# Optimization experiments

Measured on AMD Instinct MI355X. Metric: run time of the kernel, lower is better.

Reference implementation:

```python
import jax, jax.numpy as jnp
import numpy as np
from jax import lax

# static config (matches init_kwargs / input_specs)
B, T, DUR = 16, 256, 4
MEL = T * DUR                      # 1024 frames; durations rows each sum to MEL
D, H, DH, L = 512, 8, 64, 4
INTER, K, OUT = 2048, 3, 80
VOCAB, MAXLEN = 256, 4096


def _sincos(maxlen, d):
    den = jnp.exp(-jnp.arange(0, d, 2).astype(jnp.float32) * (np.log(10000.0) / d))
    ang = jnp.arange(maxlen, dtype=jnp.float32)[:, None] * den[None, :]
    return jnp.stack([jnp.sin(ang), jnp.cos(ang)], axis=-1).reshape(maxlen, d)


def _ln(x, g, b):
    m = jnp.mean(x, -1, keepdims=True)
    v = jnp.mean((x - m) ** 2, -1, keepdims=True)
    return (x - m) * lax.rsqrt(v + 1e-5) * g + b


def _layer(x, am, wqkv, bqkv, wo, bo, ln1g, ln1b, c1w, c1b, c2w, c2b, ln2g, ln2b):
    bs, s, _ = x.shape
    qkv = (x @ wqkv + bqkv).reshape(bs, s, 3, H, DH)
    q, k, v = qkv[:, :, 0], qkv[:, :, 1], qkv[:, :, 2]
    scores = jnp.einsum('bqhd,bkhd->bhqk', q, k) / np.sqrt(DH).astype(np.float32)
    scores = scores + am[:, None, None, :]          # additive key mask (-inf padded)
    attn = jax.nn.softmax(scores, axis=-1)
    ctx = jnp.einsum('bhqk,bkhd->bqhd', attn, v).reshape(bs, s, H * DH)
    x = _ln(x + ctx @ wo + bo, ln1g, ln1b)
    h = lax.conv_general_dilated(x, c1w, (1,), 'SAME', dimension_numbers=('NLC', 'LIO', 'NLC')) + c1b
    h = jax.nn.relu(h)
    h = lax.conv_general_dilated(h, c2w, (1,), 'SAME', dimension_numbers=('NLC', 'LIO', 'NLC')) + c2b
    return _ln(x + h, ln2g, ln2b)


def _stack(x, am, params):
    for i in range(L):
        x = _layer(x, am, *(p[i] for p in params))
    return x


def setup_inputs() -> dict:
    key = jax.random.key(0)
    ks = iter(jax.random.split(key, 64))

    def nrm(shape, s=0.02):
        return jax.random.normal(next(ks), shape, jnp.float32) * s

    inp = {
        'tokens': jax.random.randint(next(ks), (B, T), 0, VOCAB),
        'token_lengths': jax.random.randint(next(ks), (B,), T // 2, T),
        'melspec_length': jax.random.randint(next(ks), (B,), MEL // 2, MEL),
        'durations': jnp.full((B, T), DUR, jnp.int32),   # rows sum to MEL (module assert)
        'mel_len': MEL,
        'emb': nrm((VOCAB, D), 1.0),
    }
    for pre in ('enc', 'dec'):
        inp[pre + '_wqkv'] = nrm((L, D, 3 * H * DH))
        inp[pre + '_bqkv'] = jnp.zeros((L, 3 * H * DH))
        inp[pre + '_wo'] = nrm((L, H * DH, D))
        inp[pre + '_bo'] = jnp.zeros((L, D))
        inp[pre + '_ln1g'] = jnp.ones((L, D))
        inp[pre + '_ln1b'] = jnp.zeros((L, D))
        inp[pre + '_c1w'] = nrm((L, K, D, INTER))
        inp[pre + '_c1b'] = jnp.zeros((L, INTER))
        inp[pre + '_c2w'] = nrm((L, K, INTER, D))
        inp[pre + '_c2b'] = jnp.zeros((L, D))
        inp[pre + '_ln2g'] = jnp.ones((L, D))
        inp[pre + '_ln2b'] = jnp.zeros((L, D))
    inp['out_w'] = nrm((D, OUT))
    inp['out_b'] = jnp.zeros((OUT,))
    return inp


def reference(tokens, token_lengths, melspec_length, durations, mel_len, emb,
              enc_wqkv, enc_bqkv, enc_wo, enc_bo, enc_ln1g, enc_ln1b,
              enc_c1w, enc_c1b, enc_c2w, enc_c2b, enc_ln2g, enc_ln2b,
              dec_wqkv, dec_bqkv, dec_wo, dec_bo, dec_ln1g, dec_ln1b,
              dec_c1w, dec_c1b, dec_c2w, dec_c2b, dec_ln2g, dec_ln2b,
              out_w, out_b):
    bs, t = tokens.shape
    pos = _sincos(MAXLEAN := MAXLEN, D)
    x = emb[tokens]
    # faithful to original: x + (x + pos_embedding[:bs]) where pos buffer is [maxlen,1,D]
    x = 2.0 * x + pos[:bs][:, None, :]
    am = jnp.where(jnp.arange(t)[None, :] > token_lengths[:, None], -jnp.inf, 0.0)
    enc = _stack(x, am, (enc_wqkv, enc_bqkv, enc_wo, enc_bo, enc_ln1g, enc_ln1b,
                         enc_c1w, enc_c1b, enc_c2w, enc_c2b, enc_ln2g, enc_ln2b))
    # length regulator: equivalent gather form of mask.T @ encoder (O(MEL*D) not O(T*MEL*D))
    cums = jnp.cumsum(durations, axis=1)
    frames = jnp.arange(mel_len)
    idx = jax.vmap(lambda c: jnp.searchsorted(c, frames, side='right'))(cums)  # [B, MEL]
    dec_in = jnp.take_along_axis(enc, idx[:, :, None], axis=1)
    keep = (frames[None, :] <= melspec_length[:, None]).astype(dec_in.dtype)
    dec_in = dec_in * keep[:, :, None]
    am2 = jnp.where(frames[None, :] > melspec_length[:, None], -jnp.inf, 0.0)
    dec = _stack(dec_in, am2, (dec_wqkv, dec_bqkv, dec_wo, dec_bo, dec_ln1g, dec_ln1b,
                               dec_c1w, dec_c1b, dec_c2w, dec_c2b, dec_ln2g, dec_ln2b))
    out = dec @ out_w + out_b                      # [B, MEL, OUT]
    return jnp.transpose(out, (0, 2, 1))           # [B, OUT, MEL]
```

## Files before the change

kernel.cpp:

```cpp
#include <hip/hip_runtime.h>

typedef unsigned short u16;
typedef short short8 __attribute__((ext_vector_type(8)));
typedef float floatx4 __attribute__((ext_vector_type(4)));

static constexpr int CB = 16, CT = 256, CMEL = 1024, CD = 512, CH = 8, CDH = 64, CL = 4;
static constexpr int CINTER = 2048, COUT = 80;
static constexpr int CQKV = 3 * CH * CDH;

static __device__ __forceinline__ float bf2f(u16 u) {
  union { unsigned u; float f; } v; v.u = ((unsigned)u) << 16; return v.f;
}
static __device__ __forceinline__ u16 f2bf(float f) {
  union { float f; unsigned u; } v; v.f = f;
  unsigned r = v.u + 0x7fffu + ((v.u >> 16) & 1u);
  return (u16)(r >> 16);
}

static __device__ __forceinline__ void gld16(const u16* g, u16* lds) {
  __builtin_amdgcn_global_load_lds((const __attribute__((address_space(1))) void*)g,
                                   (__attribute__((address_space(3))) void*)lds, 16, 0, 0);
}

template<int NT, bool RELU>
__global__ __launch_bounds__(512)
void gemm2_k(const u16* __restrict__ A, const u16* __restrict__ Bm,
             u16* __restrict__ Cm, const float* __restrict__ bias,
             int M, int N, int K, int lda, int ldb, int ldc,
             int Sm1, long tapStrideB, const u16* __restrict__ zp)
{
  constexpr int BM = 256, BN = 128;
  constexpr int H = (NT == 3) ? 8 : 0;
  constexpr int AR = BM + 2 * H;
  __shared__ u16 As[AR * 32];
  __shared__ u16 Bs[NT * BN * 32];

  const int t = threadIdx.x;
  const int lane = t & 63;
  const int wave = t >> 6;
  const int wrow = wave >> 1;
  const int wcol = wave & 1;
  const int bn0 = blockIdx.x * BN;
  const int bm0 = blockIdx.y * BM;

  floatx4 acc[4][4];
#pragma unroll
  for (int i = 0; i < 4; ++i)
#pragma unroll
    for (int j = 0; j < 4; ++j) acc[i][j] = (floatx4){0.f, 0.f, 0.f, 0.f};

  const int rsub = lane >> 2;
  const int g8 = (((lane & 3) ^ ((lane >> 3) & 3)) << 3);

  const u16* aP0; const u16* aP1; const u16* aP2 = nullptr;
  {
    int gg0 = bm0 - H + wave * 16 + rsub;
    int gg1 = bm0 - H + (wave + 8) * 16 + rsub;
    aP0 = ((NT == 1) || ((unsigned)gg0 < (unsigned)M)) ? A + (long)gg0 * lda + g8 : nullptr;
    aP1 = ((NT == 1) || ((unsigned)gg1 < (unsigned)M)) ? A + (long)gg1 * lda + g8 : nullptr;
    if (NT == 3 && wave == 0) {
      int gg2 = bm0 - H + 256 + rsub;
      aP2 = ((unsigned)gg2 < (unsigned)M) ? A + (long)gg2 * lda + g8 : nullptr;
    }
  }
  const int aL0 = wave * 512, aL1 = (wave + 8) * 512, aL2 = 16 * 512;

  const u16* bP[NT]; int bL[NT];
#pragma unroll
  for (int i = 0; i < NT; ++i) {
    bP[i] = Bm + (long)i * tapStrideB + (long)(bn0 + wave * 16 + rsub) * ldb + g8;
    bL[i] = (i * BN + wave * 16) * 32;
  }

  const int q = lane >> 4, fm = lane & 15;
  const int swzB = (q ^ ((fm >> 1) & 3)) << 3;
  int swzA[NT];
  bool mv[NT][4];
#pragma unroll
  for (int tap = 0; tap < NT; ++tap) {
    const int dlt = tap - ((NT == 3) ? 1 : 0);
    swzA[tap] = (q ^ ((((H + dlt + fm) & 15) >> 1) & 3)) << 3;
#pragma unroll
    for (int i = 0; i < 4; ++i) {
      int s = (bm0 + wrow * 64 + i * 16 + fm) & Sm1;
      mv[tap][i] = ((unsigned)(s + dlt) <= (unsigned)Sm1);
    }
  }
  const short8 zero8 = {};

  for (int k0 = 0; k0 < K; k0 += 32) {
    gld16(aP0 ? aP0 + k0 : zp, &As[aL0]);
    gld16(aP1 ? aP1 + k0 : zp, &As[aL1]);
    if (NT == 3 && wave == 0) gld16(aP2 ? aP2 + k0 : zp, &As[aL2]);
#pragma unroll
    for (int i = 0; i < NT; ++i) gld16(bP[i] + k0, &Bs[bL[i]]);
    __syncthreads();

#pragma unroll
    for (int tap = 0; tap < NT; ++tap) {
      const int dlt = tap - ((NT == 3) ? 1 : 0);
      short8 af[4], bfr[4];
#pragma unroll
      for (int i = 0; i < 4; ++i) {
        af[i] = *(const short8*)&As[(wrow * 64 + i * 16 + fm + H + dlt) * 32 + swzA[tap]];
        if (NT == 3 && !mv[tap][i]) af[i] = zero8;
      }
#pragma unroll
      for (int j = 0; j < 4; ++j)
        bfr[j] = *(const short8*)&Bs[(tap * BN + wcol * 64 + j * 16 + fm) * 32 + swzB];
#pragma unroll
      for (int i = 0; i < 4; ++i)
#pragma unroll
        for (int j = 0; j < 4; ++j)
          acc[i][j] = __builtin_amdgcn_mfma_f32_16x16x32_bf16(af[i], bfr[j], acc[i][j], 0, 0, 0);
    }
    __syncthreads();
  }

  const int rbase = bm0 + wrow * 64 + ((lane >> 4) << 2);
  const int cbase = bn0 + wcol * 64 + fm;
#pragma unroll
  for (int j = 0; j < 4; ++j) {
    int col = cbase + j * 16;
    float bv = bias ? bias[col] : 0.f;
#pragma unroll
    for (int i = 0; i < 4; ++i) {
#pragma unroll
      for (int r = 0; r < 4; ++r) {
        int row = rbase + i * 16 + r;
        float v = acc[i][j][r] + bv;
        if (RELU) v = fmaxf(v, 0.f);
        Cm[(long)row * ldc + col] = f2bf(v);
      }
    }
  }
}

__global__ __launch_bounds__(512)
void attn_k(const u16* __restrict__ qkv, const u16* __restrict__ vt,
            u16* __restrict__ ctx, const int* __restrict__ lens, int S)
{
  __shared__ u16 Ks[2][64 * 32];
  __shared__ u16 Vts[2][64 * 32];
  __shared__ u16 Ps[8][16][80];

  const int t = threadIdx.x, lane = t & 63, w = t >> 6;
  const int bh = blockIdx.y, b = bh >> 3, h = bh & 7;
  const int q0 = blockIdx.x * 128;
  const int len = lens[b];
  const int fm = lane & 15, quad = lane >> 4;
  const int swz8 = ((quad ^ ((fm >> 1) & 3)) << 3);
  const int rsub = lane >> 2;
  const int g8 = (((lane & 3) ^ ((lane >> 3) & 3)) << 3);

  const int qrow = q0 + w * 16 + fm;
  short8 bq[2];
  bq[0] = *(const short8*)&qkv[(long)(b * S + qrow) * CQKV + h * 64 + quad * 8];
  bq[1] = *(const short8*)&qkv[(long)(b * S + qrow) * CQKV + h * 64 + 32 + quad * 8];

  const int ksW = w & 1, rg = (w >> 1) & 3;
  const u16* kBase = qkv + ((long)b * S + rg * 16 + rsub) * CQKV + CD + h * 64 + ksW * 32 + g8;
  const u16* vBase = vt + ((long)bh * 64 + rg * 16 + rsub) * S + ksW * 32 + g8;
  u16* kDst = &Ks[ksW][rg * 512];
  u16* vDst = &Vts[ksW][rg * 512];

  floatx4 acc_o[4];
#pragma unroll
  for (int j = 0; j < 4; ++j) acc_o[j] = (floatx4){0.f, 0.f, 0.f, 0.f};
  float m = -1e30f, l = 0.f;

  for (int kv0 = 0; kv0 < S; kv0 += 64) {
    __syncthreads();
    gld16(kBase + (long)kv0 * CQKV, kDst);
    gld16(vBase + kv0, vDst);
    __syncthreads();

    floatx4 sa[4];
#pragma unroll
    for (int i = 0; i < 4; ++i) sa[i] = (floatx4){0.f, 0.f, 0.f, 0.f};
#pragma unroll
    for (int ks = 0; ks < 2; ++ks) {
#pragma unroll
      for (int mi = 0; mi < 4; ++mi) {
        short8 ak = *(const short8*)&Ks[ks][(mi * 16 + fm) * 32 + swz8];
        sa[mi] = __builtin_amdgcn_mfma_f32_16x16x32_bf16(ak, bq[ks], sa[mi], 0, 0, 0);
      }
    }

    float p[4][4], tm = -1e30f;
#pragma unroll
    for (int mi = 0; mi < 4; ++mi)
#pragma unroll
      for (int r = 0; r < 4; ++r) {
        int kvg = kv0 + mi * 16 + quad * 4 + r;
        float v = (kvg <= len) ? sa[mi][r] * 0.125f : -1e30f;
        p[mi][r] = v; tm = fmaxf(tm, v);
      }
    tm = fmaxf(tm, __shfl_xor(tm, 16));
    tm = fmaxf(tm, __shfl_xor(tm, 32));
    const float mnew = fmaxf(m, tm);
    const float al = __expf(m - mnew);
    float ts = 0.f;
#pragma unroll
    for (int mi = 0; mi < 4; ++mi)
#pragma unroll
      for (int r = 0; r < 4; ++r) { float e = __expf(p[mi][r] - mnew); p[mi][r] = e; ts += e; }
    ts += __shfl_xor(ts, 16);
    ts += __shfl_xor(ts, 32);
    l = l * al + ts; m = mnew;
    float al4[4];
#pragma unroll
    for (int r = 0; r < 4; ++r) al4[r] = __shfl(al, ((lane >> 4) << 2) + r, 64);
#pragma unroll
    for (int j = 0; j < 4; ++j)
#pragma unroll
      for (int r = 0; r < 4; ++r) acc_o[j][r] *= al4[r];

#pragma unroll
    for (int mi = 0; mi < 4; ++mi) {
      unsigned u01 = (unsigned)f2bf(p[mi][0]) | ((unsigned)f2bf(p[mi][1]) << 16);
      unsigned u23 = (unsigned)f2bf(p[mi][2]) | ((unsigned)f2bf(p[mi][3]) << 16);
      *(uint2*)&Ps[w][fm][mi * 16 + quad * 4] = make_uint2(u01, u23);
    }

#pragma unroll
    for (int ks = 0; ks < 2; ++ks) {
      short8 ap = *(const short8*)&Ps[w][fm][ks * 32 + quad * 8];
#pragma unroll
      for (int nj = 0; nj < 4; ++nj) {
        short8 bv = *(const short8*)&Vts[ks][(nj * 16 + fm) * 32 + swz8];
        acc_o[nj] = __builtin_amdgcn_mfma_f32_16x16x32_bf16(ap, bv, acc_o[nj], 0, 0, 0);
      }
    }
  }

  float li4[4];
#pragma unroll
  for (int r = 0; r < 4; ++r) li4[r] = 1.f / __shfl(l, ((lane >> 4) << 2) + r, 64);
#pragma unroll
  for (int nj = 0; nj < 4; ++nj)
#pragma unroll
    for (int r = 0; r < 4; ++r) {
      int qr = q0 + w * 16 + quad * 4 + r;
      ctx[(long)(b * S + qr) * CD + h * 64 + nj * 16 + fm] = f2bf(acc_o[nj][r] * li4[r]);
    }
}

template<int BM, int BN>
__global__ __launch_bounds__(256)
void gemmF_k(const u16* __restrict__ A, const u16* __restrict__ Bm,
             float* __restrict__ Cm, const float* __restrict__ bias,
             int M, int N, int K, int lda, int ldb,
             const u16* __restrict__ zp)
{
  __shared__ u16 As[BM * 32];
  __shared__ u16 Bs[BN * 32];

  const int t = threadIdx.x;
  const int lane = t & 63;
  const int wave = t >> 6;
  constexpr int WCOLS = BN / 64;
  const int wrow = wave / WCOLS;
  const int wcol = wave % WCOLS;
  const int bn0 = blockIdx.x * BN;
  const int bm0 = blockIdx.y * BM;

  floatx4 acc[4][4];
#pragma unroll
  for (int i = 0; i < 4; ++i)
#pragma unroll
    for (int j = 0; j < 4; ++j) acc[i][j] = (floatx4){0.f, 0.f, 0.f, 0.f};

  const int rsub = lane >> 2;
  const int g8 = (((lane & 3) ^ ((lane >> 3) & 3)) << 3);
  constexpr int PA = BM / 64, PB = BN / 64;

  const int q = lane >> 4, fm = lane & 15;
  const int swz8 = ((q ^ ((fm >> 1) & 3)) << 3);

  const u16* aP[PA]; const u16* bP[PB];
#pragma unroll
  for (int p = 0; p < PA; ++p)
    aP[p] = A + (long)(bm0 + p * 64 + wave * 16 + rsub) * lda + g8;
#pragma unroll
  for (int p = 0; p < PB; ++p) {
    int r = p * 64 + wave * 16 + rsub;
    bP[p] = ((bn0 + r) < N) ? (Bm + (long)(bn0 + r) * ldb + g8) : nullptr;
  }

  for (int k0 = 0; k0 < K; k0 += 32) {
#pragma unroll
    for (int p = 0; p < PA; ++p)
      gld16(aP[p] + k0, &As[(p * 64 + wave * 16) * 32]);
#pragma unroll
    for (int p = 0; p < PB; ++p)
      gld16(bP[p] ? bP[p] + k0 : zp, &Bs[(p * 64 + wave * 16) * 32]);
    __syncthreads();

    short8 af[4], bfr[4];
#pragma unroll
    for (int i = 0; i < 4; ++i)
      af[i] = *(const short8*)&As[(wrow * 64 + i * 16 + fm) * 32 + swz8];
#pragma unroll
    for (int j = 0; j < 4; ++j)
      bfr[j] = *(const short8*)&Bs[(wcol * 64 + j * 16 + fm) * 32 + swz8];
#pragma unroll
    for (int i = 0; i < 4; ++i)
#pragma unroll
      for (int j = 0; j < 4; ++j)
        acc[i][j] = __builtin_amdgcn_mfma_f32_16x16x32_bf16(af[i], bfr[j], acc[i][j], 0, 0, 0);
    __syncthreads();
  }

  const int rbase = bm0 + wrow * 64 + ((lane >> 4) << 2);
  const int cbase = bn0 + wcol * 64 + (lane & 15);
#pragma unroll
  for (int j = 0; j < 4; ++j) {
    int col = cbase + j * 16;
    if (col >= N) continue;
    float bv = bias ? bias[col] : 0.f;
#pragma unroll
    for (int i = 0; i < 4; ++i) {
#pragma unroll
      for (int r = 0; r < 4; ++r) {
        int row = rbase + i * 16 + r;
        Cm[((long)(row >> 10) * COUT + col) * CMEL + (row & 1023)] = acc[i][j][r] + bv;
      }
    }
  }
}

__global__ void cvt_t_k(const float* __restrict__ src, u16* __restrict__ dst, int K, int N)
{
  const int tap = blockIdx.z;
  const int n0 = blockIdx.x * 32, k0 = blockIdx.y * 32;
  __shared__ float tile[32][33];
  const int t = threadIdx.x;
  const int c = t & 31, rr = t >> 5;
  const float* s = src + (long)tap * K * N;
  u16* d = dst + (long)tap * K * N;
#pragma unroll
  for (int i = 0; i < 4; ++i) {
    int k = k0 + rr + i * 8, n = n0 + c;
    tile[rr + i * 8][c] = (k < K && n < N) ? s[(long)k * N + n] : 0.f;
  }
  __syncthreads();
#pragma unroll
  for (int i = 0; i < 4; ++i) {
    int n = n0 + rr + i * 8, k = k0 + c;
    if (n < N && k < K) d[(long)n * K + k] = f2bf(tile[c][rr + i * 8]);
  }
}

__global__ void vtr_k(const u16* __restrict__ qkv, u16* __restrict__ vt, int S)
{
  const int s0 = blockIdx.x * 64;
  const int bh = blockIdx.y;
  const int b = bh >> 3, h = bh & 7;
  __shared__ u16 tile[64][65];
  const int t = threadIdx.x;
  const int wave = t >> 6, lane = t & 63;
#pragma unroll
  for (int i = 0; i < 16; ++i) {
    int sl = wave * 16 + i;
    tile[sl][lane] = qkv[(long)(b * S + s0 + sl) * CQKV + 2 * CD + h * 64 + lane];
  }
  __syncthreads();
  const int dl = t >> 2, sc4 = (t & 3) << 4;
  u16* dstp = vt + ((long)bh * 64 + dl) * S + s0 + sc4;
  short8 v0, v1;
#pragma unroll
  for (int j = 0; j < 8; ++j) { v0[j] = (short)tile[sc4 + j][dl]; v1[j] = (short)tile[sc4 + 8 + j][dl]; }
  *(short8*)dstp = v0;
  *(short8*)(dstp + 8) = v1;
}

__global__ void fill_k(float* __restrict__ o, int n, float v)
{
  int i = blockIdx.x * 256 + threadIdx.x;
  if (i < n) o[i] = v;
}

__global__ void embed_k(const int* __restrict__ tok, const float* __restrict__ emb,
                        u16* __restrict__ X)
{
  const long idx = (long)blockIdx.x * 256 + threadIdx.x;
  const int d = (int)(idx & (CD - 1));
  const int m = (int)(idx >> 9);
  const int b = m >> 8;
  const float e = emb[(long)tok[m] * CD + d];
  const int i2 = d >> 1;
  const float den = __expf(-(float)(2 * i2) * (9.210340371976184f / 512.f));
  const float ang = (float)b * den;
  const float p = (d & 1) ? __cosf(ang) : __sinf(ang);
  X[idx] = f2bf(2.f * e + p);
}

__global__ void ln_res_k(const u16* __restrict__ X, const u16* __restrict__ Y,
                         const float* __restrict__ g, const float* __restrict__ bta,
                         u16* __restrict__ O)
{
  const int m = blockIdx.x, t = threadIdx.x;
  const long base = (long)m * CD;
  float v0 = bf2f(X[base + t]) + bf2f(Y[base + t]);
  float v1 = bf2f(X[base + t + 256]) + bf2f(Y[base + t + 256]);
  __shared__ float red[256];
  red[t] = v0 + v1; __syncthreads();
  for (int s = 128; s > 0; s >>= 1) { if (t < s) red[t] += red[t + s]; __syncthreads(); }
  const float mean = red[0] * (1.f / 512.f);
  __syncthreads();
  const float d0 = v0 - mean, d1 = v1 - mean;
  red[t] = d0 * d0 + d1 * d1; __syncthreads();
  for (int s = 128; s > 0; s >>= 1) { if (t < s) red[t] += red[t + s]; __syncthreads(); }
  const float rstd = rsqrtf(red[0] * (1.f / 512.f) + 1e-5f);
  O[base + t]       = f2bf(d0 * rstd * g[t] + bta[t]);
  O[base + t + 256] = f2bf(d1 * rstd * g[t + 256] + bta[t + 256]);
}

__global__ void cumsum_k(const int* __restrict__ dur, int* __restrict__ cums)
{
  int b = threadIdx.x;
  if (b < CB) {
    int s = 0;
    for (int t = 0; t < CT; ++t) { s += dur[b * CT + t]; cums[b * CT + t] = s; }
  }
}

__global__ void regulate_k(const u16* __restrict__ xe, const int* __restrict__ cums,
                           const int* __restrict__ mlen, u16* __restrict__ xd)
{
  const int m = blockIdx.x;
  const int b = m >> 10, f = m & (CMEL - 1);
  int lo = 0, hi = CT;
  while (lo < hi) { int mid = (lo + hi) >> 1; if (cums[b * CT + mid] <= f) lo = mid + 1; else hi = mid; }
  const int idx = min(lo, CT - 1);
  const bool keep = (f <= mlen[b]);
  const u16* src = xe + ((long)b * CT + idx) * CD;
  u16* dst = xd + (long)m * CD;
  const int t = threadIdx.x;
  dst[t]       = keep ? src[t] : (u16)0;
  dst[t + 256] = keep ? src[t + 256] : (u16)0;
}

extern "C" void kernel_launch(void* const* d_in, const int* in_sizes, int n_in,
                              void* d_out, int out_size, void* d_ws, size_t ws_size,
                              hipStream_t stream)
{
  (void)in_sizes; (void)n_in;
  const int*   tokens = (const int*)d_in[0];
  const int*   tlen   = (const int*)d_in[1];
  const int*   mlen   = (const int*)d_in[2];
  const int*   dur    = (const int*)d_in[3];
  const float* emb    = (const float*)d_in[5];
  const float* ew[12]; const float* dw[12];
  for (int i = 0; i < 12; ++i) { ew[i] = (const float*)d_in[6 + i]; dw[i] = (const float*)d_in[18 + i]; }
  const float* out_w = (const float*)d_in[30];
  const float* out_b = (const float*)d_in[31];

  const int Me = CB * CT;
  const int Md = CB * CMEL;

  const size_t SZ_ZP   = 256;
  const size_t SZ_WBUF = (size_t)3 * CD * CINTER * 2;
  const size_t SZ_XE   = (size_t)Me * CD * 2;
  const size_t SZ_XD   = (size_t)Md * CD * 2;
  const size_t SZ_QKV  = (size_t)Md * CQKV * 2;
  const size_t SZ_HB   = (size_t)Md * CINTER * 2;
  const size_t SZ_CUMS = (size_t)CB * CT * 4;
  auto al = [](size_t b) { return (b + 255) & ~(size_t)255; };
  size_t U = al(SZ_QKV) > al(SZ_HB) ? al(SZ_QKV) : al(SZ_HB);
  size_t total = al(SZ_ZP) + al(SZ_WBUF) + al(SZ_XE) + 3 * al(SZ_XD) + U + al(SZ_CUMS);
  if (total > ws_size) {
    fill_k<<<dim3((unsigned)((out_size + 255) / 256)), dim3(256), 0, stream>>>(
        (float*)d_out, out_size, 1000.0f);
    return;
  }

  char* p = (char*)d_ws;
  auto take = [&](size_t bytes) { char* r = p; p += al(bytes); return r; };
  u16*  zp   = (u16*)take(SZ_ZP);
  u16*  wbuf = (u16*)take(SZ_WBUF);
  u16*  xe   = (u16*)take(SZ_XE);
  u16*  xd   = (u16*)take(SZ_XD);
  u16*  x1   = (u16*)take(SZ_XD);
  u16*  yb   = (u16*)take(SZ_XD);
  char* U0   = take(U);
  u16*  qkvB = (u16*)U0;
  u16*  hb   = (u16*)U0;
  int* cums = (int*)take(SZ_CUMS);

  hipMemsetAsync(zp, 0, SZ_ZP, stream);

  auto cvtT = [&](const float* s, u16* d, int K, int N, int taps) {
    cvt_t_k<<<dim3((unsigned)((N + 31) / 32), (unsigned)((K + 31) / 32), (unsigned)taps),
              dim3(256), 0, stream>>>(s, d, K, N);
  };

  embed_k<<<dim3((unsigned)((long)Me * CD / 256)), dim3(256), 0, stream>>>(tokens, emb, xe);

  auto run_stack = [&](u16* x, int S, int M, const int* lens, const float* const* W) {
    u16* vt = yb;
    for (int l = 0; l < CL; ++l) {
      cvtT(W[0] + (long)l * CD * CQKV, wbuf, CD, CQKV, 1);
      gemm2_k<1, false><<<dim3(CQKV / 128, M / 256), dim3(512), 0, stream>>>(
          x, wbuf, qkvB, W[1] + l * CQKV, M, CQKV, CD, CD, CD, CQKV, S - 1, 0, zp);
      vtr_k<<<dim3((unsigned)(S / 64), (unsigned)(CB * CH)), dim3(256), 0, stream>>>(qkvB, vt, S);
      attn_k<<<dim3((unsigned)(S / 128), (unsigned)(CB * CH)), dim3(512), 0, stream>>>(
          qkvB, vt, x1, lens, S);
      cvtT(W[2] + (long)l * CD * CD, wbuf, CD, CD, 1);
      gemm2_k<1, false><<<dim3(CD / 128, M / 256), dim3(512), 0, stream>>>(
          x1, wbuf, yb, W[3] + l * CD, M, CD, CD, CD, CD, CD, S - 1, 0, zp);
      ln_res_k<<<dim3((unsigned)M), dim3(256), 0, stream>>>(x, yb, W[4] + l * CD, W[5] + l * CD, x1);
      cvtT(W[6] + (long)l * 3 * CD * CINTER, wbuf, CD, CINTER, 3);
      gemm2_k<3, true><<<dim3(CINTER / 128, M / 256), dim3(512), 0, stream>>>(
          x1, wbuf, hb, W[7] + l * CINTER, M, CINTER, CD, CD, CD, CINTER,
          S - 1, (long)CD * CINTER, zp);
      cvtT(W[8] + (long)l * 3 * CINTER * CD, wbuf, CINTER, CD, 3);
      gemm2_k<3, false><<<dim3(CD / 128, M / 256), dim3(512), 0, stream>>>(
          hb, wbuf, yb, W[9] + l * CD, M, CD, CINTER, CINTER, CINTER, CD,
          S - 1, (long)CINTER * CD, zp);
      ln_res_k<<<dim3((unsigned)M), dim3(256), 0, stream>>>(x1, yb, W[10] + l * CD, W[11] + l * CD, x);
    }
  };

  run_stack(xe, CT, Me, tlen, ew);

  cumsum_k<<<dim3(1), dim3(64), 0, stream>>>(dur, cums);
  regulate_k<<<dim3((unsigned)(CB * CMEL)), dim3(256), 0, stream>>>(xe, cums, mlen, xd);

  run_stack(xd, CMEL, Md, mlen, dw);

  cvtT(out_w, wbuf, CD, COUT, 1);
  gemmF_k<128, 128><<<dim3(1, Md / 128), dim3(256), 0, stream>>>(
      xd, wbuf, (float*)d_out, out_b, Md, COUT, CD, CD, CD, zp);
}
```

Baseline: 2.891 ms.

## Halve GEMM row tile to 128 and widen attention KV tile to 128

The conv/projection GEMM drops from 256x128 tiles with 512 threads to 128x128 tiles with 256 threads, so each thread now loads two B rows per tap. This doubles the grid size to improve occupancy and load balance, at the cost of less A/B reuse per tile. The attention kernel now processes 128 keys per iteration instead of 64, halving the number of sync/load rounds and softmax rescales. The price is more registers per thread and larger LDS buffers.

Result: faster. 2.679 ms (-7.3%).

```diff
diff --git a/kernel.cpp b/kernel.cpp
--- a/kernel.cpp
+++ b/kernel.cpp
@@ -23,13 +23,13 @@
 }
 
 template<int NT, bool RELU>
-__global__ __launch_bounds__(512)
+__global__ __launch_bounds__(256)
 void gemm2_k(const u16* __restrict__ A, const u16* __restrict__ Bm,
              u16* __restrict__ Cm, const float* __restrict__ bias,
              int M, int N, int K, int lda, int ldb, int ldc,
              int Sm1, long tapStrideB, const u16* __restrict__ zp)
 {
-  constexpr int BM = 256, BN = 128;
+  constexpr int BM = 128, BN = 128;
   constexpr int H = (NT == 3) ? 8 : 0;
   constexpr int AR = BM + 2 * H;
   __shared__ u16 As[AR * 32];
@@ -55,22 +55,25 @@
   const u16* aP0; const u16* aP1; const u16* aP2 = nullptr;
   {
     int gg0 = bm0 - H + wave * 16 + rsub;
-    int gg1 = bm0 - H + (wave + 8) * 16 + rsub;
+    int gg1 = bm0 - H + (wave + 4) * 16 + rsub;
     aP0 = ((NT == 1) || ((unsigned)gg0 < (unsigned)M)) ? A + (long)gg0 * lda + g8 : nullptr;
     aP1 = ((NT == 1) || ((unsigned)gg1 < (unsigned)M)) ? A + (long)gg1 * lda + g8 : nullptr;
     if (NT == 3 && wave == 0) {
-      int gg2 = bm0 - H + 256 + rsub;
+      int gg2 = bm0 - H + 128 + rsub;
       aP2 = ((unsigned)gg2 < (unsigned)M) ? A + (long)gg2 * lda + g8 : nullptr;
     }
   }
-  const int aL0 = wave * 512, aL1 = (wave + 8) * 512, aL2 = 16 * 512;
-
-  const u16* bP[NT]; int bL[NT];
-#pragma unroll
-  for (int i = 0; i < NT; ++i) {
-    bP[i] = Bm + (long)i * tapStrideB + (long)(bn0 + wave * 16 + rsub) * ldb + g8;
-    bL[i] = (i * BN + wave * 16) * 32;
-  }
+  const int aL0 = wave * 512, aL1 = (wave + 4) * 512, aL2 = 8 * 512;
+
+  const u16* bP[NT][2]; int bL[NT][2];
+#pragma unroll
+  for (int i = 0; i < NT; ++i)
+#pragma unroll
+    for (int j = 0; j < 2; ++j) {
+      int r = (wave + j * 4) * 16 + rsub;
+      bP[i][j] = Bm + (long)i * tapStrideB + (long)(bn0 + r) * ldb + g8;
+      bL[i][j] = (i * BN + (wave + j * 4) * 16) * 32;
+    }
 
   const int q = lane >> 4, fm = lane & 15;
   const int swzB = (q ^ ((fm >> 1) & 3)) << 3;
@@ -93,7 +96,9 @@
     gld16(aP1 ? aP1 + k0 : zp, &As[aL1]);
     if (NT == 3 && wave == 0) gld16(aP2 ? aP2 + k0 : zp, &As[aL2]);
 #pragma unroll
-    for (int i = 0; i < NT; ++i) gld16(bP[i] + k0, &Bs[bL[i]]);
+    for (int i = 0; i < NT; ++i)
+#pragma unroll
+      for (int j = 0; j < 2; ++j) gld16(bP[i][j] + k0, &Bs[bL[i][j]]);
     __syncthreads();
 
 #pragma unroll
@@ -140,9 +145,9 @@
 void attn_k(const u16* __restrict__ qkv, const u16* __restrict__ vt,
             u16* __restrict__ ctx, const int* __restrict__ lens, int S)
 {
-  __shared__ u16 Ks[2][64 * 32];
-  __shared__ u16 Vts[2][64 * 32];
-  __shared__ u16 Ps[8][16][80];
+  __shared__ __attribute__((aligned(16))) u16 Ks[2][128 * 32];
+  __shared__ __attribute__((aligned(16))) u16 Vts[4][64 * 32];
+  __shared__ __attribute__((aligned(16))) u16 Ps[8][16][136];
 
   const int t = threadIdx.x, lane = t & 63, w = t >> 6;
   const int bh = blockIdx.y, b = bh >> 3, h = bh & 7;
@@ -158,38 +163,46 @@
   bq[0] = *(const short8*)&qkv[(long)(b * S + qrow) * CQKV + h * 64 + quad * 8];
   bq[1] = *(const short8*)&qkv[(long)(b * S + qrow) * CQKV + h * 64 + 32 + quad * 8];
 
-  const int ksW = w & 1, rg = (w >> 1) & 3;
-  const u16* kBase = qkv + ((long)b * S + rg * 16 + rsub) * CQKV + CD + h * 64 + ksW * 32 + g8;
-  const u16* vBase = vt + ((long)bh * 64 + rg * 16 + rsub) * S + ksW * 32 + g8;
-  u16* kDst = &Ks[ksW][rg * 512];
-  u16* vDst = &Vts[ksW][rg * 512];
+  const int ksW = w & 1, rgA = w >> 1, rgB = (w >> 1) + 4;
+  const u16* kBaseA = qkv + ((long)b * S + rgA * 16 + rsub) * CQKV + CD + h * 64 + ksW * 32 + g8;
+  const u16* kBaseB = qkv + ((long)b * S + rgB * 16 + rsub) * CQKV + CD + h * 64 + ksW * 32 + g8;
+  u16* kDstA = &Ks[ksW][rgA * 512];
+  u16* kDstB = &Ks[ksW][rgB * 512];
+  const int kvs0 = (2 * w) >> 2, dhc0 = (2 * w) & 3;
+  const int kvs1 = (2 * w + 1) >> 2, dhc1 = (2 * w + 1) & 3;
+  const u16* vBase0 = vt + ((long)bh * 64 + dhc0 * 16 + rsub) * S + kvs0 * 32 + g8;
+  const u16* vBase1 = vt + ((long)bh * 64 + dhc1 * 16 + rsub) * S + kvs1 * 32 + g8;
+  u16* vDst0 = &Vts[kvs0][dhc0 * 512];
+  u16* vDst1 = &Vts[kvs1][dhc1 * 512];
 
   floatx4 acc_o[4];
 #pragma unroll
   for (int j = 0; j < 4; ++j) acc_o[j] = (floatx4){0.f, 0.f, 0.f, 0.f};
   float m = -1e30f, l = 0.f;
 
-  for (int kv0 = 0; kv0 < S; kv0 += 64) {
+  for (int kv0 = 0; kv0 < S; kv0 += 128) {
     __syncthreads();
-    gld16(kBase + (long)kv0 * CQKV, kDst);
-    gld16(vBase + kv0, vDst);
+    gld16(kBaseA + (long)kv0 * CQKV, kDstA);
+    gld16(kBaseB + (long)kv0 * CQKV, kDstB);
+    gld16(vBase0 + kv0, vDst0);
+    gld16(vBase1 + kv0, vDst1);
     __syncthreads();
 
-    floatx4 sa[4];
-#pragma unroll
-    for (int i = 0; i < 4; ++i) sa[i] = (floatx4){0.f, 0.f, 0.f, 0.f};
+    floatx4 sa[8];
+#pragma unroll
+    for (int i = 0; i < 8; ++i) sa[i] = (floatx4){0.f, 0.f, 0.f, 0.f};
 #pragma unroll
     for (int ks = 0; ks < 2; ++ks) {
 #pragma unroll
-      for (int mi = 0; mi < 4; ++mi) {
+      for (int mi = 0; mi < 8; ++mi) {
         short8 ak = *(const short8*)&Ks[ks][(mi * 16 + fm) * 32 + swz8];
         sa[mi] = __builtin_amdgcn_mfma_f32_16x16x32_bf16(ak, bq[ks], sa[mi], 0, 0, 0);
       }
     }
 
-    float p[4][4], tm = -1e30f;
-#pragma unroll
-    for (int mi = 0; mi < 4; ++mi)
+    float p[8][4], tm = -1e30f;
+#pragma unroll
+    for (int mi = 0; mi < 8; ++mi)
 #pragma unroll
       for (int r = 0; r < 4; ++r) {
         int kvg = kv0 + mi * 16 + quad * 4 + r;
@@ -202,7 +215,7 @@
     const float al = __expf(m - mnew);
     float ts = 0.f;
 #pragma unroll
-    for (int mi = 0; mi < 4; ++mi)
+    for (int mi = 0; mi < 8; ++mi)
 #pragma unroll
       for (int r = 0; r < 4; ++r) { float e = __expf(p[mi][r] - mnew); p[mi][r] = e; ts += e; }
     ts += __shfl_xor(ts, 16);
@@ -217,18 +230,18 @@
       for (int r = 0; r < 4; ++r) acc_o[j][r] *= al4[r];
 
 #pragma unroll
-    for (int mi = 0; mi < 4; ++mi) {
+    for (int mi = 0; mi < 8; ++mi) {
       unsigned u01 = (unsigned)f2bf(p[mi][0]) | ((unsigned)f2bf(p[mi][1]) << 16);
       unsigned u23 = (unsigned)f2bf(p[mi][2]) | ((unsigned)f2bf(p[mi][3]) << 16);
       *(uint2*)&Ps[w][fm][mi * 16 + quad * 4] = make_uint2(u01, u23);
     }
 
 #pragma unroll
-    for (int ks = 0; ks < 2; ++ks) {
-      short8 ap = *(const short8*)&Ps[w][fm][ks * 32 + quad * 8];
+    for (int kvs = 0; kvs < 4; ++kvs) {
+      short8 ap = *(const short8*)&Ps[w][fm][kvs * 32 + quad * 8];
 #pragma unroll
       for (int nj = 0; nj < 4; ++nj) {
-        short8 bv = *(const short8*)&Vts[ks][(nj * 16 + fm) * 32 + swz8];
+        short8 bv = *(const short8*)&Vts[kvs][(nj * 16 + fm) * 32 + swz8];
         acc_o[nj] = __builtin_amdgcn_mfma_f32_16x16x32_bf16(ap, bv, acc_o[nj], 0, 0, 0);
       }
     }
@@ -502,21 +515,21 @@
     u16* vt = yb;
     for (int l = 0; l < CL; ++l) {
       cvtT(W[0] + (long)l * CD * CQKV, wbuf, CD, CQKV, 1);
-      gemm2_k<1, false><<<dim3(CQKV / 128, M / 256), dim3(512), 0, stream>>>(
+      gemm2_k<1, false><<<dim3(CQKV / 128, M / 128), dim3(256), 0, stream>>>(
           x, wbuf, qkvB, W[1] + l * CQKV, M, CQKV, CD, CD, CD, CQKV, S - 1, 0, zp);
       vtr_k<<<dim3((unsigned)(S / 64), (unsigned)(CB * CH)), dim3(256), 0, stream>>>(qkvB, vt, S);
       attn_k<<<dim3((unsigned)(S / 128), (unsigned)(CB * CH)), dim3(512), 0, stream>>>(
           qkvB, vt, x1, lens, S);
       cvtT(W[2] + (long)l * CD * CD, wbuf, CD, CD, 1);
-      gemm2_k<1, false><<<dim3(CD / 128, M / 256), dim3(512), 0, stream>>>(
+      gemm2_k<1, false><<<dim3(CD / 128, M / 128), dim3(256), 0, stream>>>(
           x1, wbuf, yb, W[3] + l * CD, M, CD, CD, CD, CD, CD, S - 1, 0, zp);
       ln_res_k<<<dim3((unsigned)M), dim3(256), 0, stream>>>(x, yb, W[4] + l * CD, W[5] + l * CD, x1);
       cvtT(W[6] + (long)l * 3 * CD * CINTER, wbuf, CD, CINTER, 3);
-      gemm2_k<3, true><<<dim3(CINTER / 128, M / 256), dim3(512), 0, stream>>>(
+      gemm2_k<3, true><<<dim3(CINTER / 128, M / 128), dim3(256), 0, stream>>>(
           x1, wbuf, hb, W[7] + l * CINTER, M, CINTER, CD, CD, CD, CINTER,
           S - 1, (long)CD * CINTER, zp);
       cvtT(W[8] + (long)l * 3 * CINTER * CD, wbuf, CINTER, CD, 3);
-      gemm2_k<3, false><<<dim3(CD / 128, M / 256), dim3(512), 0, stream>>>(
+      gemm2_k<3, false><<<dim3(CD / 128, M / 128), dim3(256), 0, stream>>>(
           hb, wbuf, yb, W[9] + l * CD, M, CD, CINTER, CINTER, CINTER, CD,
           S - 1, (long)CINTER * CD, zp);
       ln_res_k<<<dim3((unsigned)M), dim3(256), 0, stream>>>(x1, yb, W[10] + l * CD, W[11] + l * CD, x);
```
